# Kernel tuning notes

Measured on AMD Instinct MI355X. Metric: run time of the kernel, lower is better.

The kernel has to match this reference:

```python
import jax, jax.numpy as jnp
import numpy as np

SQRT_N = 64  # sqrt_n; padded sequence length n = SQRT_N**2 = 4096


def _perm(x, r):
    # rearrange '... (m n) -> ... (n m)' with m = n = r
    return x.reshape(*x.shape[:-1], r, r).swapaxes(-1, -2).reshape(x.shape)


def _blockdiag_matmul(x, w):
    # torch.einsum('bnm,...bm->...bn', w, x.view(..., b, m)).reshape(x.shape)
    b, _, m = w.shape
    xv = x.reshape(*x.shape[:-1], b, m)
    return jnp.einsum('bnm,...bm->...bn', w, xv).reshape(x.shape)


def _monarch(x, L, R, r):
    x = _perm(x, r)
    x = _blockdiag_matmul(x, L)
    x = _perm(x, r)
    x = _blockdiag_matmul(x, R)
    return _perm(x, r)


def setup_inputs() -> dict:
    key = jax.random.key(0)
    ks = jax.random.split(key, 9)
    B, S, H, D = 8, 4096, 8, 64
    r = SQRT_N
    bound_b = 1.0 / r
    # kaiming_uniform_(a=sqrt(5)) on a (r, r, r) tensor: fan_in = r*r,
    # gain = sqrt(2/(1+5)) = sqrt(1/3), bound = gain*sqrt(3/fan_in) = 1/r
    bound_w = 1.0 / r
    return {
        'queries': jax.random.normal(ks[0], (B, S, H, D), jnp.float32),
        'keys': jax.random.normal(ks[1], (B, S, H, D), jnp.float32),
        'values': jax.random.normal(ks[2], (B, S, H, D), jnp.float32),
        'M1L': jax.random.uniform(ks[3], (r, r, r), jnp.float32, -bound_w, bound_w),
        'M1R': jax.random.uniform(ks[4], (r, r, r), jnp.float32, -bound_w, bound_w),
        'M2L': jax.random.uniform(ks[5], (r, r, r), jnp.float32, -bound_w, bound_w),
        'M2R': jax.random.uniform(ks[6], (r, r, r), jnp.float32, -bound_w, bound_w),
        'b1': jax.random.uniform(ks[7], (r * r,), jnp.float32, -bound_b, bound_b),
        'b2': jax.random.uniform(ks[8], (r * r,), jnp.float32, -bound_b, bound_b),
    }


def reference(queries, keys, values, M1L, M1R, M2L, M2R, b1, b2):
    r = SQRT_N
    B, S, H, D = queries.shape
    n2 = r * r
    pad = n2 - S
    # (B,S,H,D) -> (B,H,D,S)
    q = jnp.transpose(queries, (0, 2, 3, 1))
    k = jnp.transpose(keys, (0, 2, 3, 1))
    v = jnp.transpose(values, (0, 2, 3, 1))
    cfg = [(0, 0)] * 3 + [(0, pad)]
    q = jnp.pad(q, cfg)
    k = jnp.pad(k, cfg)
    # A = M1(q) * k + b1 ; dropout is identity (eval / p=0)
    A = _monarch(q, M1L, M1R, r) * k + b1
    A = _monarch(A, M2L, M2R, r) + b2
    Y = A[..., :S] * v  # (B,H,D,S)
    return Y
```

## Files before the change

### kernel.cpp

```cpp
#include <hip/hip_runtime.h>
#include <cstdint>
#include <cstddef>

typedef unsigned short u16;
typedef __attribute__((ext_vector_type(8))) short bf16x8;
typedef __attribute__((ext_vector_type(4))) float f32x4;

#define S_LEN 4096

__device__ __forceinline__ float bf2f(u16 u) {
  return __uint_as_float(((unsigned)u) << 16);
}
__device__ __forceinline__ u16 f2bf(float f) {
  unsigned x = __float_as_uint(f);
  return (u16)((x + 0x7fffu + ((x >> 16) & 1u)) >> 16);
}
__device__ __forceinline__ unsigned pk2(float a, float b) {
  unsigned r;
  asm("v_cvt_pk_bf16_f32 %0, %1, %2" : "=v"(r) : "v"(a), "v"(b));
  return r;
}

__device__ __forceinline__ int tst(int r, int x) {
  return ((x >> 4) << 10) + ((r >> 5) << 9) + (((r >> 2) & 1) << 8) +
         (((r >> 3) & 3) << 6) + ((r & 3) << 4) + (x & 15);
}
__device__ __forceinline__ int rdig(int r) {
  return ((r >> 5) << 9) + (((r >> 2) & 1) << 8) + (((r >> 3) & 3) << 6) + ((r & 3) << 4);
}

__device__ __forceinline__ uint2 trr(const ushort* p) {
  uint2 d;
  asm volatile("ds_read_b64_tr_b16 %0, %1" : "=v"(d) : "v"((unsigned)(uintptr_t)p));
  return d;
}

__device__ __forceinline__ bf16x8 apk_frag(const u16* __restrict__ APK, int mat, int gr,
                                           int ks, int lane) {
  return *(const bf16x8*)&APK[(((((mat << 8) + gr) << 1) + ks) << 9) + lane * 8];
}

__device__ __forceinline__ int ltelem(int c, int r) {
  int swz = ((r >> 3) ^ (c & 7) ^ ((c >> 3) & 7)) & 7;
  return (c << 6) | (swz << 3) | (r & 7);
}
__device__ __forceinline__ bf16x8 tile_frag(const ushort* LT, int a, int ks, int lane) {
  int c = (a << 4) + (lane & 15);
  int kg = (ks << 2) + (lane >> 4);
  int base = (c << 6) | (((kg ^ (c & 7) ^ ((c >> 3) & 7)) & 7) << 3);
  return *(const bf16x8*)&LT[base];
}
__device__ __forceinline__ void mmT_old(const ushort* LT, const u16* __restrict__ APK,
                                        int mat, int gr, int lane, f32x4 acc[4]) {
#pragma unroll
  for (int ks = 0; ks < 2; ++ks) {
    bf16x8 bw = apk_frag(APK, mat, gr, ks, lane);
#pragma unroll
    for (int a = 0; a < 4; ++a) {
      bf16x8 at = tile_frag(LT, a, ks, lane);
      acc[a] = __builtin_amdgcn_mfma_f32_16x16x32_bf16(at, bw, acc[a], 0, 0, 0);
    }
  }
}

__device__ __forceinline__ void mmT_tr(const ushort* LT, const u16* __restrict__ APK,
                                       int mat, int gr, int lane, f32x4 acc[4]) {
  const ushort* base = LT + ((lane & 15) + ((lane >> 4) << 6));
  uint2 fr[4][2][2];
#pragma unroll
  for (int a = 0; a < 4; ++a)
#pragma unroll
    for (int ks = 0; ks < 2; ++ks)
#pragma unroll
      for (int eh = 0; eh < 2; ++eh)
        fr[a][ks][eh] = trr(base + (a << 10) + (ks << 9) + (eh << 8));
  asm volatile("s_waitcnt lgkmcnt(0)" ::: "memory");
  __builtin_amdgcn_sched_barrier(0);
#pragma unroll
  for (int ks = 0; ks < 2; ++ks) {
    bf16x8 bw = apk_frag(APK, mat, gr, ks, lane);
#pragma unroll
    for (int a = 0; a < 4; ++a) {
      union { uint2 u[2]; bf16x8 v; } cv;
      cv.u[0] = fr[a][ks][0];
      cv.u[1] = fr[a][ks][1];
      acc[a] = __builtin_amdgcn_mfma_f32_16x16x32_bf16(cv.v, bw, acc[a], 0, 0, 0);
    }
  }
}

__global__ __launch_bounds__(256) void k_prep(const float* __restrict__ W0,
                                              const float* __restrict__ W1,
                                              const float* __restrict__ W2,
                                              const float* __restrict__ W3,
                                              u16* __restrict__ APK) {
  const int gr = blockIdx.x, mat = blockIdx.y;
  const float* W = (mat == 0) ? W0 : (mat == 1) ? W1 : (mat == 2) ? W2 : W3;
  const int t = threadIdx.x;
  const int lane = t & 63, ks = (t >> 6) & 1, half = t >> 7;
  const int row = gr * 16 + (lane & 15);
  const int k0 = ks * 32 + ((lane >> 4) << 3) + half * 4;
  float4 v = *(const float4*)&W[row * 64 + k0];
  ushort4 o;
  o.x = f2bf(v.x); o.y = f2bf(v.y); o.z = f2bf(v.z); o.w = f2bf(v.w);
  *(ushort4*)&APK[((((((mat << 8) + gr) << 1) + ks) << 6) + lane) * 8 + half * 4] = o;
}

__global__ __launch_bounds__(256) void k_m1(const float* __restrict__ q,
                                            const u16* __restrict__ APK,
                                            u16* __restrict__ T1) {
  const int B = blockIdx.x, bh = blockIdx.y;
  const int b = bh >> 3, h = bh & 7;
  __shared__ __align__(16) ushort LT[4096];
  const int tid = threadIdx.x, w = tid >> 6, lane = tid & 63;
  {
    const int m = tid >> 2, ch = tid & 3;
    const float* qrow = q + ((((size_t)b * S_LEN + (size_t)m * 64 + B) * 8 + h) << 6);
#pragma unroll
    for (int i = 0; i < 4; ++i) {
      float4 v = *(const float4*)(qrow + ch * 16 + i * 4);
      int c0 = ch * 16 + i * 4;
      LT[ltelem(c0 + 0, m)] = f2bf(v.x);
      LT[ltelem(c0 + 1, m)] = f2bf(v.y);
      LT[ltelem(c0 + 2, m)] = f2bf(v.z);
      LT[ltelem(c0 + 3, m)] = f2bf(v.w);
    }
  }
  __syncthreads();
  f32x4 acc[4] = {};
  mmT_old(LT, APK, 0, B * 4 + w, lane, acc);
  const int n = (w << 4) + (lane & 15);
  const int dg = (lane >> 4) << 2;
  const int Bd = rdig(B);
  u16* dst = T1 + (((size_t)bh * 64 + n) << 12);
#pragma unroll
  for (int a = 0; a < 4; ++a) {
    ushort4 o;
    o.x = f2bf(acc[a][0]); o.y = f2bf(acc[a][1]);
    o.z = f2bf(acc[a][2]); o.w = f2bf(acc[a][3]);
    *(ushort4*)&dst[(a << 10) + Bd + dg] = o;
  }
}

__global__ __launch_bounds__(256) void k_m2b(const u16* __restrict__ T1,
                                             const u16* __restrict__ APK,
                                             const float* __restrict__ keys,
                                             const float* __restrict__ b1,
                                             u16* __restrict__ T2) {
  const int n = blockIdx.x, bh = blockIdx.y;
  const int b = bh >> 3, h = bh & 7;
  __shared__ __align__(16) ushort LT[4096];
  __shared__ __align__(16) ushort LT2[4096];
  const int tid = threadIdx.x, w = tid >> 6, lane = tid & 63;
  const int p = (w << 4) + (lane & 15);
  const int dg = (lane >> 4) << 2;

  const float b1v = b1[p * 64 + n];
  const float* krow = &keys[(((size_t)b * S_LEN + p * 64 + n) * 8 + h) << 6];
  float4 kreg[4];
#pragma unroll
  for (int a = 0; a < 4; ++a) kreg[a] = *(const float4*)(krow + (a << 4) + dg);

  {
    const uint4* src = (const uint4*)(T1 + (((size_t)bh * 64 + n) << 12));
    uint4 v0 = src[tid], v1 = src[tid + 256];
    ((uint4*)LT)[tid] = v0;
    ((uint4*)LT)[tid + 256] = v1;
  }
  __syncthreads();

  f32x4 acc[4] = {};
  mmT_tr(LT, APK, 1, n * 4 + w, lane, acc);
  const int pd = rdig(p);
#pragma unroll
  for (int a = 0; a < 4; ++a) {
    uint2 pw;
    pw.x = pk2(acc[a][0] * kreg[a].x + b1v, acc[a][1] * kreg[a].y + b1v);
    pw.y = pk2(acc[a][2] * kreg[a].z + b1v, acc[a][3] * kreg[a].w + b1v);
    *(uint2*)&LT2[(a << 10) + pd + dg] = pw;
  }
  __syncthreads();

  f32x4 acc2[4] = {};
  mmT_tr(LT2, APK, 2, n * 4 + w, lane, acc2);
  const int nd = rdig(n);
  u16* dst = T2 + (((size_t)bh * 64 + p) << 12);
#pragma unroll
  for (int a = 0; a < 4; ++a) {
    ushort4 o;
    o.x = f2bf(acc2[a][0]); o.y = f2bf(acc2[a][1]);
    o.z = f2bf(acc2[a][2]); o.w = f2bf(acc2[a][3]);
    *(ushort4*)&dst[(a << 10) + nd + dg] = o;
  }
}

__global__ __launch_bounds__(256) void k_m3b(const u16* __restrict__ T2,
                                             const u16* __restrict__ APK,
                                             const float* __restrict__ vals,
                                             const float* __restrict__ b2,
                                             u16* __restrict__ Yp) {
  const int np = blockIdx.x, bh = blockIdx.y;
  const int b = bh >> 3, h = bh & 7;
  __shared__ __align__(16) ushort LT[4096];
  const int tid = threadIdx.x, w = tid >> 6, lane = tid & 63;
  const int p = (w << 4) + (lane & 15);
  const int dg = (lane >> 4) << 2;

  const float b2v = b2[p * 64 + np];
  const float* vrow = &vals[(((size_t)b * S_LEN + p * 64 + np) * 8 + h) << 6];
  float4 vreg[4];
#pragma unroll
  for (int a = 0; a < 4; ++a) vreg[a] = *(const float4*)(vrow + (a << 4) + dg);

  {
    const uint4* src = (const uint4*)(T2 + (((size_t)bh * 64 + np) << 12));
    uint4 v0 = src[tid], v1 = src[tid + 256];
    ((uint4*)LT)[tid] = v0;
    ((uint4*)LT)[tid + 256] = v1;
  }
  __syncthreads();

  f32x4 acc[4] = {};
  mmT_tr(LT, APK, 3, np * 4 + w, lane, acc);
#pragma unroll
  for (int a = 0; a < 4; ++a) {
    int d0 = (a << 4) + dg;
    ushort4 o;
    o.x = f2bf((acc[a][0] + b2v) * vreg[a].x);
    o.y = f2bf((acc[a][1] + b2v) * vreg[a].y);
    o.z = f2bf((acc[a][2] + b2v) * vreg[a].z);
    o.w = f2bf((acc[a][3] + b2v) * vreg[a].w);
    *(ushort4*)&Yp[(((size_t)bh * 64 + np) * 64 + p) * 64 + d0] = o;
  }
}

__global__ __launch_bounds__(256) void k_tr(const u16* __restrict__ Yp,
                                            float* __restrict__ out) {
  const int p = blockIdx.x, bh = blockIdx.y;
  __shared__ __align__(16) ushort YT[4096];
  const int tid = threadIdx.x;
#pragma unroll
  for (int i = 0; i < 2; ++i) {
    int idx = i * 256 + tid;
    int np = idx >> 3, q8 = idx & 7;
    uint4 vv = *(const uint4*)&Yp[(((size_t)bh * 64 + np) * 64 + p) * 64 + q8 * 8];
    *(uint4*)&YT[ltelem(np, q8 * 8)] = vv;
  }
  __syncthreads();
#pragma unroll
  for (int i = 0; i < 4; ++i) {
    int idx = i * 256 + tid;
    int d = idx >> 4, np0 = (idx & 15) * 4;
    float4 o;
    o.x = bf2f(YT[ltelem(np0 + 0, d)]);
    o.y = bf2f(YT[ltelem(np0 + 1, d)]);
    o.z = bf2f(YT[ltelem(np0 + 2, d)]);
    o.w = bf2f(YT[ltelem(np0 + 3, d)]);
    *(float4*)&out[((size_t)bh * 64 + d) * S_LEN + p * 64 + np0] = o;
  }
}

extern "C" void kernel_launch(void* const* d_in, const int* in_sizes, int n_in,
                              void* d_out, int out_size, void* d_ws, size_t ws_size,
                              hipStream_t stream) {
  const float* q   = (const float*)d_in[0];
  const float* k   = (const float*)d_in[1];
  const float* v   = (const float*)d_in[2];
  const float* M1L = (const float*)d_in[3];
  const float* M1R = (const float*)d_in[4];
  const float* M2L = (const float*)d_in[5];
  const float* M2R = (const float*)d_in[6];
  const float* b1  = (const float*)d_in[7];
  const float* b2  = (const float*)d_in[8];

  u16* T1 = (u16*)d_ws;
  u16* T2 = T1 + (size_t)64 * 64 * 64 * 64;
  u16* Yp = T1;
  u16* APK = (u16*)d_out;

  dim3 blk(256);
  dim3 grd(64, 64);
  k_prep<<<dim3(256, 4), blk, 0, stream>>>(M1L, M1R, M2L, M2R, APK);
  k_m1 <<<grd, blk, 0, stream>>>(q, APK, T1);
  k_m2b<<<grd, blk, 0, stream>>>(T1, APK, k, b1, T2);
  k_m3b<<<grd, blk, 0, stream>>>(T2, APK, v, b2, Yp);
  k_tr <<<grd, blk, 0, stream>>>(Yp, (float*)d_out);
}
```

Before: 118.6 us.

## Vectorize k_m1 LDS staging with transpose reads and process two n per m2b block

k_m1 now packs q rows to bf16 with v_cvt_pk and writes 16-byte chunks into the rdig-swizzled LDS layout. This replaces scalar per-element swizzled stores, and the MFMA operands are read with ds_read_b64_tr_b16 instead of the old swizzled fragment loads. k_m2b handles two n columns per block with doubled LDS buffers, issuing all global loads up front for more memory-level parallelism, and its grid is halved. The cost is doubled shared memory and register use in k_m2b, which may lower occupancy.

```diff
diff --git a/kernel.cpp b/kernel.cpp
--- a/kernel.cpp
+++ b/kernel.cpp
@@ -21,10 +21,6 @@
   return r;
 }
 
-__device__ __forceinline__ int tst(int r, int x) {
-  return ((x >> 4) << 10) + ((r >> 5) << 9) + (((r >> 2) & 1) << 8) +
-         (((r >> 3) & 3) << 6) + ((r & 3) << 4) + (x & 15);
-}
 __device__ __forceinline__ int rdig(int r) {
   return ((r >> 5) << 9) + (((r >> 2) & 1) << 8) + (((r >> 3) & 3) << 6) + ((r & 3) << 4);
 }
@@ -38,29 +34,6 @@
 __device__ __forceinline__ bf16x8 apk_frag(const u16* __restrict__ APK, int mat, int gr,
                                            int ks, int lane) {
   return *(const bf16x8*)&APK[(((((mat << 8) + gr) << 1) + ks) << 9) + lane * 8];
-}
-
-__device__ __forceinline__ int ltelem(int c, int r) {
-  int swz = ((r >> 3) ^ (c & 7) ^ ((c >> 3) & 7)) & 7;
-  return (c << 6) | (swz << 3) | (r & 7);
-}
-__device__ __forceinline__ bf16x8 tile_frag(const ushort* LT, int a, int ks, int lane) {
-  int c = (a << 4) + (lane & 15);
-  int kg = (ks << 2) + (lane >> 4);
-  int base = (c << 6) | (((kg ^ (c & 7) ^ ((c >> 3) & 7)) & 7) << 3);
-  return *(const bf16x8*)&LT[base];
-}
-__device__ __forceinline__ void mmT_old(const ushort* LT, const u16* __restrict__ APK,
-                                        int mat, int gr, int lane, f32x4 acc[4]) {
-#pragma unroll
-  for (int ks = 0; ks < 2; ++ks) {
-    bf16x8 bw = apk_frag(APK, mat, gr, ks, lane);
-#pragma unroll
-    for (int a = 0; a < 4; ++a) {
-      bf16x8 at = tile_frag(LT, a, ks, lane);
-      acc[a] = __builtin_amdgcn_mfma_f32_16x16x32_bf16(at, bw, acc[a], 0, 0, 0);
-    }
-  }
 }
 
 __device__ __forceinline__ void mmT_tr(const ushort* LT, const u16* __restrict__ APK,
@@ -87,6 +60,11 @@
       acc[a] = __builtin_amdgcn_mfma_f32_16x16x32_bf16(cv.v, bw, acc[a], 0, 0, 0);
     }
   }
+}
+
+__device__ __forceinline__ int ltelem(int c, int r) {
+  int swz = ((r >> 3) ^ (c & 7) ^ ((c >> 3) & 7)) & 7;
+  return (c << 6) | (swz << 3) | (r & 7);
 }
 
 __global__ __launch_bounds__(256) void k_prep(const float* __restrict__ W0,
@@ -115,22 +93,25 @@
   const int tid = threadIdx.x, w = tid >> 6, lane = tid & 63;
   {
     const int m = tid >> 2, ch = tid & 3;
-    const float* qrow = q + ((((size_t)b * S_LEN + (size_t)m * 64 + B) * 8 + h) << 6);
-#pragma unroll
-    for (int i = 0; i < 4; ++i) {
-      float4 v = *(const float4*)(qrow + ch * 16 + i * 4);
-      int c0 = ch * 16 + i * 4;
-      LT[ltelem(c0 + 0, m)] = f2bf(v.x);
-      LT[ltelem(c0 + 1, m)] = f2bf(v.y);
-      LT[ltelem(c0 + 2, m)] = f2bf(v.z);
-      LT[ltelem(c0 + 3, m)] = f2bf(v.w);
-    }
+    const float* qrow = q + ((((size_t)b * S_LEN + (size_t)m * 64 + B) * 8 + h) << 6) + ch * 16;
+    float4 v0 = ((const float4*)qrow)[0];
+    float4 v1 = ((const float4*)qrow)[1];
+    float4 v2 = ((const float4*)qrow)[2];
+    float4 v3 = ((const float4*)qrow)[3];
+    uint4 p0, p1;
+    p0.x = pk2(v0.x, v0.y); p0.y = pk2(v0.z, v0.w);
+    p0.z = pk2(v1.x, v1.y); p0.w = pk2(v1.z, v1.w);
+    p1.x = pk2(v2.x, v2.y); p1.y = pk2(v2.z, v2.w);
+    p1.z = pk2(v3.x, v3.y); p1.w = pk2(v3.z, v3.w);
+    u16* dst = LT + (ch << 10) + rdig(m);
+    *(uint4*)dst = p0;
+    *(uint4*)(dst + 8) = p1;
   }
   __syncthreads();
   f32x4 acc[4] = {};
-  mmT_old(LT, APK, 0, B * 4 + w, lane, acc);
+  mmT_tr(LT, APK, 0, B * 4 + w, lane, acc);
+  const int dg = (lane >> 4) << 2;
   const int n = (w << 4) + (lane & 15);
-  const int dg = (lane >> 4) << 2;
   const int Bd = rdig(B);
   u16* dst = T1 + (((size_t)bh * 64 + n) << 12);
 #pragma unroll
@@ -147,50 +128,65 @@
                                              const float* __restrict__ keys,
                                              const float* __restrict__ b1,
                                              u16* __restrict__ T2) {
-  const int n = blockIdx.x, bh = blockIdx.y;
+  const int n0 = blockIdx.x << 1, bh = blockIdx.y;
   const int b = bh >> 3, h = bh & 7;
-  __shared__ __align__(16) ushort LT[4096];
-  __shared__ __align__(16) ushort LT2[4096];
+  __shared__ __align__(16) ushort LT[2][4096];
+  __shared__ __align__(16) ushort LT2[2][4096];
   const int tid = threadIdx.x, w = tid >> 6, lane = tid & 63;
   const int p = (w << 4) + (lane & 15);
   const int dg = (lane >> 4) << 2;
 
-  const float b1v = b1[p * 64 + n];
-  const float* krow = &keys[(((size_t)b * S_LEN + p * 64 + n) * 8 + h) << 6];
-  float4 kreg[4];
-#pragma unroll
-  for (int a = 0; a < 4; ++a) kreg[a] = *(const float4*)(krow + (a << 4) + dg);
-
+  uint4 s00, s01, s10, s11;
   {
-    const uint4* src = (const uint4*)(T1 + (((size_t)bh * 64 + n) << 12));
-    uint4 v0 = src[tid], v1 = src[tid + 256];
-    ((uint4*)LT)[tid] = v0;
-    ((uint4*)LT)[tid + 256] = v1;
-  }
-  __syncthreads();
-
-  f32x4 acc[4] = {};
-  mmT_tr(LT, APK, 1, n * 4 + w, lane, acc);
+    const uint4* src0 = (const uint4*)(T1 + (((size_t)bh * 64 + n0) << 12));
+    const uint4* src1 = (const uint4*)(T1 + (((size_t)bh * 64 + n0 + 1) << 12));
+    s00 = src0[tid]; s01 = src0[tid + 256];
+    s10 = src1[tid]; s11 = src1[tid + 256];
+  }
+  float4 kreg[2][4];
+  float b1v[2];
+#pragma unroll
+  for (int t = 0; t < 2; ++t) {
+    const int n = n0 + t;
+    b1v[t] = b1[p * 64 + n];
+    const float* krow = &keys[(((size_t)b * S_LEN + p * 64 + n) * 8 + h) << 6];
+#pragma unroll
+    for (int a = 0; a < 4; ++a) kreg[t][a] = *(const float4*)(krow + (a << 4) + dg);
+  }
+  ((uint4*)LT[0])[tid] = s00; ((uint4*)LT[0])[tid + 256] = s01;
+  ((uint4*)LT[1])[tid] = s10; ((uint4*)LT[1])[tid + 256] = s11;
+  __syncthreads();
+
   const int pd = rdig(p);
 #pragma unroll
-  for (int a = 0; a < 4; ++a) {
-    uint2 pw;
-    pw.x = pk2(acc[a][0] * kreg[a].x + b1v, acc[a][1] * kreg[a].y + b1v);
-    pw.y = pk2(acc[a][2] * kreg[a].z + b1v, acc[a][3] * kreg[a].w + b1v);
-    *(uint2*)&LT2[(a << 10) + pd + dg] = pw;
-  }
-  __syncthreads();
-
-  f32x4 acc2[4] = {};
-  mmT_tr(LT2, APK, 2, n * 4 + w, lane, acc2);
-  const int nd = rdig(n);
+  for (int t = 0; t < 2; ++t) {
+    const int n = n0 + t;
+    f32x4 acc[4] = {};
+    mmT_tr(LT[t], APK, 1, n * 4 + w, lane, acc);
+#pragma unroll
+    for (int a = 0; a < 4; ++a) {
+      uint2 pw;
+      pw.x = pk2(acc[a][0] * kreg[t][a].x + b1v[t], acc[a][1] * kreg[t][a].y + b1v[t]);
+      pw.y = pk2(acc[a][2] * kreg[t][a].z + b1v[t], acc[a][3] * kreg[t][a].w + b1v[t]);
+      *(uint2*)&LT2[t][(a << 10) + pd + dg] = pw;
+    }
+  }
+  __syncthreads();
+
   u16* dst = T2 + (((size_t)bh * 64 + p) << 12);
 #pragma unroll
-  for (int a = 0; a < 4; ++a) {
-    ushort4 o;
-    o.x = f2bf(acc2[a][0]); o.y = f2bf(acc2[a][1]);
-    o.z = f2bf(acc2[a][2]); o.w = f2bf(acc2[a][3]);
-    *(ushort4*)&dst[(a << 10) + nd + dg] = o;
+  for (int t = 0; t < 2; ++t) {
+    const int n = n0 + t;
+    f32x4 acc2[4] = {};
+    mmT_tr(LT2[t], APK, 2, n * 4 + w, lane, acc2);
+    const int nd = rdig(n);
+#pragma unroll
+    for (int a = 0; a < 4; ++a) {
+      ushort4 o;
+      o.x = f2bf(acc2[a][0]); o.y = f2bf(acc2[a][1]);
+      o.z = f2bf(acc2[a][2]); o.w = f2bf(acc2[a][3]);
+      *(ushort4*)&dst[(a << 10) + nd + dg] = o;
+    }
   }
 }
 
@@ -279,10 +275,9 @@
   u16* APK = (u16*)d_out;
 
   dim3 blk(256);
-  dim3 grd(64, 64);
   k_prep<<<dim3(256, 4), blk, 0, stream>>>(M1L, M1R, M2L, M2R, APK);
-  k_m1 <<<grd, blk, 0, stream>>>(q, APK, T1);
-  k_m2b<<<grd, blk, 0, stream>>>(T1, APK, k, b1, T2);
-  k_m3b<<<grd, blk, 0, stream>>>(T2, APK, v, b2, Yp);
-  k_tr <<<grd, blk, 0, stream>>>(Yp, (float*)d_out);
-}
+  k_m1 <<<dim3(64, 64), blk, 0, stream>>>(q, APK, T1);
+  k_m2b<<<dim3(32, 64), blk, 0, stream>>>(T1, APK, k, b1, T2);
+  k_m3b<<<dim3(64, 64), blk, 0, stream>>>(T2, APK, v, b2, Yp);
+  k_tr <<<dim3(64, 64), blk, 0, stream>>>(Yp, (float*)d_out);
+}
```

After: 115.0 us. -3.1%, faster.
